# Kernel tuning notes

Measured on AMD Instinct MI355X. Metric: run time of the kernel, lower is better.

Reference implementation:

```python
import jax, jax.numpy as jnp
import numpy as np

B, S = 4, 16384
D_IN, D_HID, D_KEY, D_VAL, N_HEADS = 512, 2048, 64, 64, 8
SEG_FULL, SAMP = 2048, 4
SEG = SEG_FULL // SAMP  # 512: MoD capacity per segment, also attn segment_len


def setup_inputs() -> dict:
    key = jax.random.key(0)
    ks = jax.random.split(key, 10)
    sc = lambda i, shape: (jax.random.normal(ks[i], shape, jnp.float32) * 0.02)
    return {
        "x": jax.random.normal(ks[0], (B, S, D_IN), jnp.float32),
        "w_samp": sc(1, (D_IN, 1)), "b_samp": jnp.zeros((1,), jnp.float32),
        "w_q": sc(2, (D_IN, N_HEADS * D_KEY)),
        "w_k": sc(3, (D_IN, N_HEADS * D_KEY)),
        "w_v": sc(4, (D_IN, N_HEADS * D_VAL)),
        "w_o": sc(5, (N_HEADS * D_VAL, D_IN)),
        "betas": jax.random.normal(ks[6], (1, N_HEADS, 1, D_VAL), jnp.float32),
        "w1": sc(7, (D_IN, D_HID)), "b1": jnp.zeros((D_HID,), jnp.float32),
        "w2": sc(8, (D_HID, D_IN)), "b2": jnp.zeros((D_IN,), jnp.float32),
    }


def _cm_attention(x, w_q, w_k, w_v, w_o, betas):
    """CompressiveMemory: segment-recurrent linear-attn memory + local softmax attn."""
    b, n, _ = x.shape
    nseg = n // SEG

    def split(w, dh):
        y = (x @ w).reshape(b, n, N_HEADS, dh).transpose(0, 2, 1, 3)          # [b,H,n,dh]
        return y.reshape(b, N_HEADS, nseg, SEG, dh).transpose(2, 0, 1, 3, 4)  # [nseg,b,H,SEG,dh]

    qs, ks_, vs = split(w_q, D_KEY), split(w_k, D_KEY), split(w_v, D_VAL)
    gate = jax.nn.sigmoid(betas)                                              # [1,H,1,dv]
    mem0 = jnp.zeros((b, N_HEADS, D_KEY, D_VAL), x.dtype)
    z0 = jnp.ones((b, N_HEADS, D_KEY, 1), x.dtype) / D_KEY
    scale = D_KEY ** -0.5

    def step(carry, seg):
        mem, z = carry
        q, k, v = seg
        sq = jax.nn.elu(q) + 1.0
        sk = jax.nn.elu(k) + 1.0
        scores = jnp.einsum('bhqk,bhsk->bhqs', q, k) * scale
        att_dot = jax.nn.softmax(scores, axis=-1) @ v                         # [b,H,SEG,dv]
        att_mem = (sq @ mem) / (sq @ z)                                       # uses pre-update mem,z
        mem = mem + jnp.einsum('bhsk,bhsv->bhkv', sk, v)                      # linear update
        z = z + sk.sum(axis=-2)[..., None]
        att = gate * att_mem + (1.0 - gate) * att_dot
        return (mem, z), att

    _, outs = jax.lax.scan(step, (mem0, z0), (qs, ks_, vs))                   # [nseg,b,H,SEG,dv]
    out = outs.transpose(1, 0, 3, 2, 4).reshape(b, n, N_HEADS * D_VAL)
    return out @ w_o


def reference(x, w_samp, b_samp, w_q, w_k, w_v, w_o, betas, w1, b1, w2, b2):
    b, s, d = x.shape
    nseg = s // SEG_FULL
    scores = (x @ w_samp + b_samp)[..., 0]                                    # [B,S]
    # top-SEG tokens per full segment (training-mode routing), kept in sequence order
    seg_scores = scores.reshape(b, nseg, SEG_FULL)
    top = jnp.argsort(-seg_scores, axis=-1)[:, :, :SEG]                       # [B,nseg,SEG]
    sel = jnp.sort(top, axis=-1) + (jnp.arange(nseg) * SEG_FULL)[None, :, None]
    flat = sel.reshape(b, nseg * SEG)                                         # global indices, [B,Ssel]
    x_sel = jnp.take_along_axis(x, flat[..., None], axis=1)                   # gather [B,Ssel,D]
    h = _cm_attention(x_sel, w_q, w_k, w_v, w_o, betas)
    h = jax.nn.gelu(h @ w1 + b1, approximate=False) @ w2 + b2                 # MLP (dropout=0)
    bi = jnp.arange(b)[:, None]
    x_out = x.at[bi, flat].add(h)                                             # scatter-add back
    mask = jnp.zeros((b, s), x.dtype).at[bi, flat].set(1.0)
    # faithful to source: zero positions >= number of selected tokens
    pad = (jnp.arange(s)[None, :] < mask.sum(axis=1)[:, None]).astype(x.dtype)
    x_out = x_out * pad[..., None]
    return x_out, mask.reshape(-1, 1), scores.reshape(-1, 1)
```

## Files before the change

### kernel.cpp

```cpp
#include <hip/hip_runtime.h>
#include <math.h>

#define S_TOT 16384
#define BATCH 4
#define DIN 512
#define NH 8
#define DK 64
#define SEGF 2048
#define SEGS 512
#define NSEG 8
#define NUSE 2
#define MROWS (BATCH*NUSE*SEGS)

typedef unsigned int u32;
typedef __attribute__((ext_vector_type(8))) short short8;
typedef __attribute__((ext_vector_type(4))) float f32x4;

__device__ __forceinline__ short f2b(float f) {
  u32 u = __float_as_uint(f);
  u32 r = u + 0x7fffu + ((u >> 16) & 1u);
  return (short)(r >> 16);
}
__device__ __forceinline__ float b2f(short s) {
  return __uint_as_float(((u32)(unsigned short)s) << 16);
}

__global__ __launch_bounds__(256) void scores_transpose(
    const float* __restrict__ x, const float* __restrict__ w,
    const float* __restrict__ bsamp, float* __restrict__ out,
    const float* __restrict__ w_q, const float* __restrict__ w_k,
    const float* __restrict__ w_v, const float* __restrict__ w_o,
    const float* __restrict__ w1,  const float* __restrict__ w2,
    short* __restrict__ Wtqkv, short* __restrict__ Wob,
    short* __restrict__ Wt1,   short* __restrict__ Wt2)
{
  __shared__ float t[32][33];
  int tid = threadIdx.x;
  if (blockIdx.x < 16384) {
    int tok  = blockIdx.x * 4 + (tid >> 6);
    int lane = tid & 63;
    const float4* xr = (const float4*)(x + (size_t)tok * DIN);
    const float4* wr = (const float4*)w;
    float4 a0 = xr[lane],      w0 = wr[lane];
    float4 a1 = xr[lane + 64], w1v = wr[lane + 64];
    float p = a0.x*w0.x + a0.y*w0.y + a0.z*w0.z + a0.w*w0.w
            + a1.x*w1v.x + a1.y*w1v.y + a1.z*w1v.z + a1.w*w1v.w;
    #pragma unroll
    for (int off = 32; off > 0; off >>= 1) p += __shfl_down(p, off);
    if (lane == 0) out[tok] = p + bsamp[0];
    return;
  }
  int bid = blockIdx.x - 16384;
  int txx = tid & 31, ty = tid >> 5;
  if (bid >= 768 && bid < 1024) {
    int tIdx = bid - 768;
    int n0 = (tIdx & 15) * 32, k0 = (tIdx >> 4) * 32;
    #pragma unroll
    for (int r = 0; r < 4; ++r) {
      size_t idx = (size_t)(k0 + ty + 8*r) * 512 + n0 + txx;
      Wob[idx] = f2b(w_o[idx]);
    }
    return;
  }
  const float* src; short* dst; int K, N, rowoff, tIdx;
  if (bid < 768) {
    K = 512; N = 512; tIdx = bid & 255;
    int which = bid >> 8;
    src = which == 0 ? w_q : which == 1 ? w_k : w_v;
    dst = Wtqkv;
    rowoff = which * 512;
  } else if (bid < 2048) {
    K = 512; N = 2048; tIdx = bid - 1024; src = w1; dst = Wt1; rowoff = 0;
  } else {
    K = 2048; N = 512; tIdx = bid - 2048; src = w2; dst = Wt2; rowoff = 0;
  }
  int ntN = N >> 5;
  int n0 = (tIdx % ntN) * 32, k0 = (tIdx / ntN) * 32;
  #pragma unroll
  for (int r = 0; r < 4; ++r)
    t[ty + 8*r][txx] = src[(size_t)(k0 + ty + 8*r) * N + n0 + txx];
  __syncthreads();
  #pragma unroll
  for (int r = 0; r < 4; ++r)
    dst[(size_t)(rowoff + n0 + ty + 8*r) * K + k0 + txx] = f2b(t[txx][ty + 8*r]);
}

__global__ __launch_bounds__(1024) void topk_rank(
    const float* __restrict__ scores, int* __restrict__ flags,
    float* __restrict__ maskOut)
{
  int c = blockIdx.x & 7, g = (blockIdx.x >> 3) & 7, b = blockIdx.x >> 6;
  __shared__ float sc[SEGF];
  __shared__ int pcnt[3][256];
  int tid = threadIdx.x;
  const float* src = scores + (size_t)b*S_TOT + (size_t)g*SEGF;
  *(float2*)&sc[tid*2] = *(const float2*)(src + tid*2);
  __syncthreads();
  int e = tid & 255;
  int q = tid >> 8;
  int i0 = c*256 + e;
  float mine = sc[i0];
  int cnt = 0;
  int j0 = q * 512;
  #pragma unroll 2
  for (int j = j0; j < j0 + 512; j += 8) {
    float4 a = *(const float4*)&sc[j];
    float4 d = *(const float4*)&sc[j + 4];
    cnt += (a.x > mine || (a.x == mine && (j+0) < i0)) ? 1 : 0;
    cnt += (a.y > mine || (a.y == mine && (j+1) < i0)) ? 1 : 0;
    cnt += (a.z > mine || (a.z == mine && (j+2) < i0)) ? 1 : 0;
    cnt += (a.w > mine || (a.w == mine && (j+3) < i0)) ? 1 : 0;
    cnt += (d.x > mine || (d.x == mine && (j+4) < i0)) ? 1 : 0;
    cnt += (d.y > mine || (d.y == mine && (j+5) < i0)) ? 1 : 0;
    cnt += (d.z > mine || (d.z == mine && (j+6) < i0)) ? 1 : 0;
    cnt += (d.w > mine || (d.w == mine && (j+7) < i0)) ? 1 : 0;
  }
  if (q) pcnt[q-1][e] = cnt;
  __syncthreads();
  if (q == 0) {
    cnt += pcnt[0][e] + pcnt[1][e] + pcnt[2][e];
    int flg = (cnt < SEGS) ? 1 : 0;
    flags[(((b << 3) + g) << 11) + i0] = flg;
    maskOut[(size_t)b*S_TOT + (size_t)g*SEGF + i0] = flg ? 1.0f : 0.0f;
  }
}

__global__ __launch_bounds__(256) void topk_compact(
    const int* __restrict__ flags, int* __restrict__ flat, int* __restrict__ inv)
{
  int g = blockIdx.x & 1, b = blockIdx.x >> 1;
  __shared__ int wsum[4];
  int tid = threadIdx.x;
  int lane = tid & 63, w = tid >> 6;
  const int* f = flags + (((b << 3) + g) << 11);
  int fl[8]; int ls = 0;
  #pragma unroll
  for (int l = 0; l < 8; ++l) { fl[l] = f[tid*8 + l]; ls += fl[l]; }
  int inc = ls;
  #pragma unroll
  for (int off = 1; off < 64; off <<= 1) {
    int t = __shfl_up(inc, off);
    if (lane >= off) inc += t;
  }
  if (lane == 63) wsum[w] = inc;
  __syncthreads();
  int base = 0;
  #pragma unroll
  for (int ww = 0; ww < 4; ++ww) base += (ww < w) ? wsum[ww] : 0;
  int pos = base + inc - ls;
  #pragma unroll
  for (int l = 0; l < 8; ++l) {
    int i = tid*8 + l;
    inv[b*(NUSE*SEGF) + g*SEGF + i] = fl[l] ? (g*SEGS + pos) : -1;
    if (fl[l]) {
      flat[b*(NSEG*SEGS) + g*SEGS + pos] = g*SEGF + i;
      pos++;
    }
  }
}

__global__ __launch_bounds__(256) void gather_cast(
    const float* __restrict__ x, const int* __restrict__ flat,
    short* __restrict__ xsel)
{
  int tok  = blockIdx.x * 4 + (threadIdx.x >> 6);
  int lane = threadIdx.x & 63;
  int b = tok >> 10, i = tok & 1023;
  int gidx = flat[b * (NSEG*SEGS) + i];
  const float* srcp = x + ((size_t)(b * S_TOT + gidx)) * DIN + lane*8;
  float4 a0 = *(const float4*)srcp;
  float4 a1 = *(const float4*)(srcp + 4);
  uint4 o;
  o.x = (u32)(unsigned short)f2b(a0.x) | ((u32)(unsigned short)f2b(a0.y) << 16);
  o.y = (u32)(unsigned short)f2b(a0.z) | ((u32)(unsigned short)f2b(a0.w) << 16);
  o.z = (u32)(unsigned short)f2b(a1.x) | ((u32)(unsigned short)f2b(a1.y) << 16);
  o.w = (u32)(unsigned short)f2b(a1.z) | ((u32)(unsigned short)f2b(a1.w) << 16);
  *(uint4*)(xsel + (size_t)tok * DIN + lane*8) = o;
}

template<int BM, int BN, int WM, int WN, int BK>
__global__ __launch_bounds__(256) void gemm_bf16(
    const short* __restrict__ A, const short* __restrict__ Bt,
    const float* __restrict__ bias, float* __restrict__ Cf,
    short* __restrict__ Cb, short* __restrict__ VtOut, short* __restrict__ KtOut,
    int M, int N, int K, int act)
{
  constexpr int WAVES_N = BN / WN;
  constexpr int FM = WM / 16, FN = WN / 16;
  constexpr int RPB = BK / 8;
  __shared__ short Al[2][BM * BK];
  __shared__ short Bl[2][BN * BK];
  const int tid = threadIdx.x;
  const int lane = tid & 63, wid = tid >> 6;
  const int wr = wid / WAVES_N, wc = wid % WAVES_N;
  const int bm = blockIdx.y * BM, bn = blockIdx.x * BN;
  const int ln15 = lane & 15, hi8 = (lane >> 4) * 8;

  f32x4 acc[FM][FN];
  #pragma unroll
  for (int i = 0; i < FM; ++i)
    #pragma unroll
    for (int j = 0; j < FN; ++j)
      #pragma unroll
      for (int e = 0; e < 4; ++e) acc[i][j][e] = 0.f;

  const int NT = K / BK;

  auto stage = [&](int t, int buf) {
    const int k0 = t * BK;
    #pragma unroll
    for (int i = 0; i < BM*BK/2048; ++i) {
      int slot = i*256 + tid;
      int row = slot / RPB, col = (slot % RPB) * 8;
      const short* gp = A + (size_t)(bm + row) * K + k0 + col;
      __builtin_amdgcn_global_load_lds(
          (const __attribute__((address_space(1))) void*)gp,
          (__attribute__((address_space(3))) void*)&Al[buf][row*BK + col],
          16, 0, 0);
    }
    #pragma unroll
    for (int i = 0; i < BN*BK/2048; ++i) {
      int slot = i*256 + tid;
      int row = slot / RPB, col = (slot % RPB) * 8;
      const short* gp = Bt + (size_t)(bn + row) * K + k0 + col;
      __builtin_amdgcn_global_load_lds(
          (const __attribute__((address_space(1))) void*)gp,
          (__attribute__((address_space(3))) void*)&Bl[buf][row*BK + col],
          16, 0, 0);
    }
  };

  stage(0, 0);
  __syncthreads();
  int cur = 0;
  for (int t = 0; t < NT; ++t) {
    if (t + 1 < NT) stage(t + 1, cur ^ 1);
    #pragma unroll
    for (int ks = 0; ks < BK/32; ++ks) {
      short8 af[FM], bf_[FN];
      #pragma unroll
      for (int fm = 0; fm < FM; ++fm)
        af[fm] = *(const short8*)&Al[cur][(wr*WM + fm*16 + ln15)*BK + ks*32 + hi8];
      #pragma unroll
      for (int fn = 0; fn < FN; ++fn)
        bf_[fn] = *(const short8*)&Bl[cur][(wc*WN + fn*16 + ln15)*BK + ks*32 + hi8];
      #pragma unroll
      for (int fm = 0; fm < FM; ++fm)
        #pragma unroll
        for (int fn = 0; fn < FN; ++fn)
          acc[fm][fn] = __builtin_amdgcn_mfma_f32_16x16x32_bf16(af[fm], bf_[fn], acc[fm][fn], 0, 0, 0);
    }
    __syncthreads();
    cur ^= 1;
  }

  const int crow0 = (lane >> 4) * 4, ccol = lane & 15;
  #pragma unroll
  for (int fm = 0; fm < FM; ++fm) {
    #pragma unroll
    for (int fn = 0; fn < FN; ++fn) {
      int c = bn + wc*WN + fn*16 + ccol;
      int r0 = bm + wr*WM + fm*16 + crow0;
      float vv[4];
      #pragma unroll
      for (int j = 0; j < 4; ++j) {
        float v = acc[fm][fn][j];
        if (bias) v += bias[c];
        if (act == 1) v = 0.5f * v * (1.0f + erff(v * 0.70710678118f));
        vv[j] = v;
        if (Cf) Cf[(size_t)(r0 + j) * N + c] = v;
        if (Cb) Cb[(size_t)(r0 + j) * N + c] = f2b(v);
      }
      if (VtOut && c >= 1024) {
        int hh = (c - 1024) >> 6, dv = c & 63;
        int bb = r0 >> 10, key = r0 & 1023;
        u32 lo = (u32)(unsigned short)f2b(vv[0]) | ((u32)(unsigned short)f2b(vv[1]) << 16);
        u32 hi = (u32)(unsigned short)f2b(vv[2]) | ((u32)(unsigned short)f2b(vv[3]) << 16);
        *(uint2*)&VtOut[((size_t)((bb*8 + hh)*64 + dv) << 10) + key] = make_uint2(lo, hi);
      }
      if (KtOut && c >= 512 && c < 1024) {
        int hh = (c - 512) >> 6, dk = c & 63;
        int bb = r0 >> 10, key = r0 & 1023;
        float e0 = vv[0] > 0.f ? vv[0] + 1.f : __expf(vv[0]);
        float e1 = vv[1] > 0.f ? vv[1] + 1.f : __expf(vv[1]);
        float e2 = vv[2] > 0.f ? vv[2] + 1.f : __expf(vv[2]);
        float e3 = vv[3] > 0.f ? vv[3] + 1.f : __expf(vv[3]);
        u32 lo = (u32)(unsigned short)f2b(e0) | ((u32)(unsigned short)f2b(e1) << 16);
        u32 hi = (u32)(unsigned short)f2b(e2) | ((u32)(unsigned short)f2b(e3) << 16);
        *(uint2*)&KtOut[((size_t)((bb*8 + hh)*64 + dk) << 10) + key] = make_uint2(lo, hi);
      }
    }
  }
}

__global__ __launch_bounds__(256) void memsum_mfma(
    const short* __restrict__ Kt, const short* __restrict__ Vt,
    short* __restrict__ m0t, float* __restrict__ zf)
{
  int b = blockIdx.x >> 3, h = blockIdx.x & 7;
  const short* ktb = Kt + ((size_t)((b*8+h)*64) << 10);
  const short* vtb = Vt + ((size_t)((b*8+h)*64) << 10);
  int tid = threadIdx.x, lane = tid & 63, w = tid >> 6;
  int ln15 = lane & 15, hi8 = (lane >> 4) * 8;
  f32x4 acc[4];
  #pragma unroll
  for (int nf = 0; nf < 4; ++nf) acc[nf] = (f32x4){0.f,0.f,0.f,0.f};
  #pragma unroll 4
  for (int ks = 0; ks < 16; ++ks) {
    short8 a = *(const short8*)&vtb[(size_t)(w*16 + ln15)*1024 + ks*32 + hi8];
    #pragma unroll
    for (int nf = 0; nf < 4; ++nf) {
      short8 bfr = *(const short8*)&ktb[(size_t)(nf*16 + ln15)*1024 + ks*32 + hi8];
      acc[nf] = __builtin_amdgcn_mfma_f32_16x16x32_bf16(a, bfr, acc[nf], 0, 0, 0);
    }
  }
  size_t mb = (size_t)(b*NH + h) * 4096;
  #pragma unroll
  for (int nf = 0; nf < 4; ++nf)
    #pragma unroll
    for (int j = 0; j < 4; ++j)
      m0t[mb + (size_t)(w*16 + (lane>>4)*4 + j)*64 + nf*16 + ln15] = f2b(acc[nf][j]);
  int row = tid >> 2, q = tid & 3;
  float zs = 0.f;
  #pragma unroll 4
  for (int i = 0; i < 16; ++i) {
    short8 kv = *(const short8*)&ktb[(size_t)row*1024 + q*128 + i*8];
    #pragma unroll
    for (int e = 0; e < 8; ++e) zs += b2f(kv[e]);
  }
  zs += __shfl_xor(zs, 1); zs += __shfl_xor(zs, 2);
  if (q == 0) zf[(b*8+h)*64 + row] = 0.015625f + zs;
}

__global__ __launch_bounds__(256) void attn4(
    const short* __restrict__ qkv, const short* __restrict__ vt,
    const short* __restrict__ m0t, const float* __restrict__ zf,
    const float* __restrict__ betas, short* __restrict__ att)
{
  __shared__ short Ks[128*64];
  __shared__ short Vts[64*128];
  __shared__ short Ps[4*16*128];
  __shared__ float zl[64];
  __shared__ float relay[64];
  int tid = threadIdx.x, lane = tid & 63, w = tid >> 6;
  int ln15 = lane & 15, hi8 = (lane >> 4) * 8;
  int bx = blockIdx.x;
  int qt = bx & 7, h = (bx >> 3) & 7, g = (bx >> 6) & 1, b = bx >> 7;
  const int seg0 = b*1024 + g*512;
  const int qbase = seg0 + qt*64;

  short8 qf[2];
  {
    const short* qg = qkv + (size_t)(qbase + w*16 + ln15)*1536 + h*64;
    qf[0] = *(const short8*)(qg + hi8);
    qf[1] = *(const short8*)(qg + 32 + hi8);
  }
  if (g && tid < 16) *(float4*)&zl[tid*4] = *(const float4*)(zf + (size_t)(b*8+h)*64 + tid*4);

  const short* kg = qkv + (size_t)seg0*1536 + 512 + h*64;
  const short* vg = vt + ((size_t)((b*8+h)*64) << 10) + g*512;
  short* Pw = &Ps[w*2048];

  f32x4 oacc[4];
  #pragma unroll
  for (int nf = 0; nf < 4; ++nf) oacc[nf] = (f32x4){0.f,0.f,0.f,0.f};
  float lsum[4] = {0.f,0.f,0.f,0.f};

  for (int c = 0; c < 4; ++c) {
    __syncthreads();
    #pragma unroll
    for (int p = 0; p < 4; ++p) {
      int slot = p*256 + tid;
      int row = slot >> 3;
      int off = ((slot & 7)*8) ^ ((row & 7)*8);
      __builtin_amdgcn_global_load_lds(
        (const __attribute__((address_space(1))) void*)(kg + (size_t)(c*128 + row)*1536 + off),
        (__attribute__((address_space(3))) void*)&Ks[slot*8], 16, 0, 0);
    }
    #pragma unroll
    for (int p = 0; p < 4; ++p) {
      int slot = p*256 + tid;
      int row = slot >> 4;
      int off = ((slot & 15)*8) ^ ((row & 7)*8);
      __builtin_amdgcn_global_load_lds(
        (const __attribute__((address_space(1))) void*)(vg + ((size_t)row << 10) + c*128 + off),
        (__attribute__((address_space(3))) void*)&Vts[slot*8], 16, 0, 0);
    }
    __syncthreads();

    f32x4 sf[8];
    #pragma unroll
    for (int nf = 0; nf < 8; ++nf) sf[nf] = (f32x4){0.f,0.f,0.f,0.f};
    __builtin_amdgcn_s_setprio(1);
    #pragma unroll
    for (int ks = 0; ks < 2; ++ks)
      #pragma unroll
      for (int nf = 0; nf < 8; ++nf) {
        int row = nf*16 + ln15;
        short8 kb = *(const short8*)&Ks[row*64 + ((ks*32 + hi8) ^ ((row&7)*8))];
        sf[nf] = __builtin_amdgcn_mfma_f32_16x16x32_bf16(qf[ks], kb, sf[nf], 0, 0, 0);
      }
    __builtin_amdgcn_s_setprio(0);
    #pragma unroll
    for (int nf = 0; nf < 8; ++nf)
      #pragma unroll
      for (int j = 0; j < 4; ++j) {
        float p = __expf(sf[nf][j] * 0.125f);
        lsum[j] += p;
        int q = (lane >> 4)*4 + j;
        int key = nf*16 + ln15;
        Pw[q*128 + (key ^ ((q&7)*8))] = f2b(p);
      }
    __builtin_amdgcn_s_setprio(1);
    #pragma unroll
    for (int ks = 0; ks < 4; ++ks) {
      short8 pa = *(const short8*)&Pw[ln15*128 + ((ks*32 + hi8) ^ ((ln15&7)*8))];
      #pragma unroll
      for (int nf = 0; nf < 4; ++nf) {
        int row = nf*16 + ln15;
        short8 vb = *(const short8*)&Vts[row*128 + ((ks*32 + hi8) ^ ((row&7)*8))];
        oacc[nf] = __builtin_amdgcn_mfma_f32_16x16x32_bf16(pa, vb, oacc[nf], 0, 0, 0);
      }
    }
    __builtin_amdgcn_s_setprio(0);
  }

  float linv[4];
  #pragma unroll
  for (int j = 0; j < 4; ++j) {
    float s = lsum[j];
    s += __shfl_xor(s, 1); s += __shfl_xor(s, 2);
    s += __shfl_xor(s, 4); s += __shfl_xor(s, 8);
    linv[j] = 1.f / s;
  }

  f32x4 mfr[4];
  #pragma unroll
  for (int nf = 0; nf < 4; ++nf) mfr[nf] = (f32x4){0.f,0.f,0.f,0.f};
  float dinv[4] = {0.f,0.f,0.f,0.f};
  if (g) {
    __syncthreads();
    const short* mg = m0t + (size_t)(b*8+h)*4096;
    #pragma unroll
    for (int p = 0; p < 2; ++p) {
      int slot = p*256 + tid;
      int row = slot >> 3;
      int off = ((slot & 7)*8) ^ ((row & 7)*8);
      __builtin_amdgcn_global_load_lds(
        (const __attribute__((address_space(1))) void*)(mg + (size_t)row*64 + off),
        (__attribute__((address_space(3))) void*)&Ks[slot*8], 16, 0, 0);
    }
    __syncthreads();
    float sqv[2][8]; short8 sqf[2];
    #pragma unroll
    for (int ks = 0; ks < 2; ++ks)
      #pragma unroll
      for (int e = 0; e < 8; ++e) {
        float f = b2f(qf[ks][e]);
        f = f > 0.f ? f + 1.f : __expf(f);
        sqv[ks][e] = f; sqf[ks][e] = f2b(f);
      }
    float denp = 0.f;
    #pragma unroll
    for (int ks = 0; ks < 2; ++ks)
      #pragma unroll
      for (int e = 0; e < 8; ++e) denp += sqv[ks][e] * zl[ks*32 + hi8 + e];
    denp += __shfl_xor(denp, 16); denp += __shfl_xor(denp, 32);
    if (lane < 16) relay[w*16 + lane] = denp;
    #pragma unroll
    for (int ks = 0; ks < 2; ++ks)
      #pragma unroll
      for (int nf = 0; nf < 4; ++nf) {
        int row = nf*16 + ln15;
        short8 mb_ = *(const short8*)&Ks[row*64 + ((ks*32 + hi8) ^ ((row&7)*8))];
        mfr[nf] = __builtin_amdgcn_mfma_f32_16x16x32_bf16(sqf[ks], mb_, mfr[nf], 0, 0, 0);
      }
    #pragma unroll
    for (int j = 0; j < 4; ++j)
      dinv[j] = 1.f / relay[w*16 + (lane>>4)*4 + j];
  }

  #pragma unroll
  for (int nf = 0; nf < 4; ++nf) {
    float bt = betas[h*64 + nf*16 + ln15];
    float gt = 1.f / (1.f + __expf(-bt));
    #pragma unroll
    for (int j = 0; j < 4; ++j) {
      float ad = oacc[nf][j] * linv[j];
      float v = g ? (gt * mfr[nf][j] * dinv[j] + (1.f - gt) * ad) : (1.f - gt) * ad;
      int qrow = qbase + w*16 + (lane>>4)*4 + j;
      att[(size_t)qrow*512 + h*64 + nf*16 + ln15] = f2b(v);
    }
  }
}

__global__ __launch_bounds__(256) void final_kernel(
    const float* __restrict__ x, const int* __restrict__ inv,
    const float* __restrict__ hm, float* __restrict__ outX)
{
  int row  = blockIdx.x * 4 + (threadIdx.x >> 6);
  int lane = threadIdx.x & 63;
  int b = row >> 14;
  int s = row & (S_TOT - 1);
  size_t base = (size_t)row * DIN + lane * 8;
  if (s >= NUSE * SEGF) {
    float4 z = make_float4(0.f,0.f,0.f,0.f);
    *(float4*)(outX + base)     = z;
    *(float4*)(outX + base + 4) = z;
    return;
  }
  float4 a0 = *(const float4*)(x + base);
  float4 a1 = *(const float4*)(x + base + 4);
  int i = inv[b * (NUSE*SEGF) + s];
  if (i >= 0) {
    size_t hb = (size_t)(b * (NUSE*SEGS) + i) * DIN + lane * 8;
    float4 h0 = *(const float4*)(hm + hb);
    float4 h1 = *(const float4*)(hm + hb + 4);
    a0.x += h0.x; a0.y += h0.y; a0.z += h0.z; a0.w += h0.w;
    a1.x += h1.x; a1.y += h1.y; a1.z += h1.z; a1.w += h1.w;
  }
  *(float4*)(outX + base)     = a0;
  *(float4*)(outX + base + 4) = a1;
}

extern "C" void kernel_launch(void* const* d_in, const int* in_sizes, int n_in,
                              void* d_out, int out_size, void* d_ws, size_t ws_size,
                              hipStream_t stream) {
  (void)in_sizes; (void)n_in; (void)out_size; (void)ws_size;
  const float* x      = (const float*)d_in[0];
  const float* w_samp = (const float*)d_in[1];
  const float* b_samp = (const float*)d_in[2];
  const float* w_q    = (const float*)d_in[3];
  const float* w_k    = (const float*)d_in[4];
  const float* w_v    = (const float*)d_in[5];
  const float* w_o    = (const float*)d_in[6];
  const float* betas  = (const float*)d_in[7];
  const float* w1     = (const float*)d_in[8];
  const float* b1     = (const float*)d_in[9];
  const float* w2     = (const float*)d_in[10];
  const float* b2     = (const float*)d_in[11];

  float* outX      = (float*)d_out;
  float* outMask   = outX + (size_t)BATCH * S_TOT * DIN;
  float* outScores = outMask + (size_t)BATCH * S_TOT;

  char* ws = (char*)d_ws;
  int*   flat  = (int*)(ws);
  int*   inv   = (int*)(ws + 65536);
  int*   flags = (int*)(ws + 131072);
  short* M0t   = (short*)(ws + 393216);
  float* Zf    = (float*)(ws + 655360);
  short* Wtqkv = (short*)(ws + 1048576);
  short* Wob   = (short*)(ws + 2621440);
  short* Wt1   = (short*)(ws + 3145728);
  short* Wt2   = (short*)(ws + 5242880);
  short* xsel  = (short*)(ws + 7340032);
  short* qkv   = (short*)(ws + 11534336);
  short* Vt    = (short*)(ws + 24117248);
  short* attb  = (short*)(ws + 28311552);
  short* Kt    = (short*)(ws + 36700160);
  short* WfT   = (short*)(ws + 40894464);
  short* hidB  = (short*)(ws + 7340032);
  float* Hf    = (float*)(ws + 24117248);

  scores_transpose<<<16384 + 3072, 256, 0, stream>>>(
      x, w_samp, b_samp, outScores,
      w_q, w_k, w_v, w_o, w1, w2, Wtqkv, Wob, Wt1, Wt2);
  topk_rank<<<BATCH*NSEG*8, 1024, 0, stream>>>(outScores, flags, outMask);
  topk_compact<<<BATCH*NUSE, 256, 0, stream>>>(flags, flat, inv);

  gemm_bf16<64,64,32,32,64><<<dim3(8,32), 256, 0, stream>>>(
      Wt1, Wob, nullptr, nullptr, WfT, nullptr, nullptr, 2048, 512, 512, 0);

  gather_cast<<<MROWS/4, 256, 0, stream>>>(x, flat, xsel);

  gemm_bf16<128,128,64,64,32><<<dim3(12,32), 256, 0, stream>>>(
      xsel, Wtqkv, nullptr, nullptr, qkv, Vt, Kt, MROWS, 1536, 512, 0);

  memsum_mfma<<<BATCH*NH, 256, 0, stream>>>(Kt, Vt, M0t, Zf);
  attn4<<<512, 256, 0, stream>>>(qkv, Vt, M0t, Zf, betas, attb);

  gemm_bf16<128,128,64,64,32><<<dim3(16,32), 256, 0, stream>>>(
      attb, WfT, b1, nullptr, hidB, nullptr, nullptr, MROWS, 2048, 512, 1);
  gemm_bf16<64,64,32,32,64><<<dim3(8,64), 256, 0, stream>>>(
      hidB, Wt2, b2, Hf, nullptr, nullptr, nullptr, MROWS, 512, 2048, 0);

  final_kernel<<<(BATCH*S_TOT)/4, 256, 0, stream>>>(x, inv, Hf, outX);
}
```

Measured before the change: 218.8 us.

## Fuse residual scatter into final GEMM and memory summary into attention

Removes the separate final_kernel and Hf buffer. The last MLP GEMM now writes x plus h directly into the output rows given by the gather indices, and the gather kernel copies unselected rows and zeroes padded rows. It also removes the memsum_mfma launch by having each second-segment attention block recompute the per-head memory matrix and normalizer from Kt/Vt into LDS. This saves launches and a full-size pass over the intermediate, but the memory matrix is now computed redundantly by 8 query-tile blocks per head, and the epilogue does scattered, per-element residual reads.

Result: slower. 227.9 us (+4.2%).

```diff
diff --git a/kernel.cpp b/kernel.cpp
--- a/kernel.cpp
+++ b/kernel.cpp
@@ -159,23 +159,41 @@
   }
 }
 
-__global__ __launch_bounds__(256) void gather_cast(
+__global__ __launch_bounds__(256) void gather_base(
     const float* __restrict__ x, const int* __restrict__ flat,
-    short* __restrict__ xsel)
+    const int* __restrict__ inv, short* __restrict__ xsel,
+    float* __restrict__ outX)
 {
-  int tok  = blockIdx.x * 4 + (threadIdx.x >> 6);
-  int lane = threadIdx.x & 63;
-  int b = tok >> 10, i = tok & 1023;
-  int gidx = flat[b * (NSEG*SEGS) + i];
-  const float* srcp = x + ((size_t)(b * S_TOT + gidx)) * DIN + lane*8;
-  float4 a0 = *(const float4*)srcp;
-  float4 a1 = *(const float4*)(srcp + 4);
-  uint4 o;
-  o.x = (u32)(unsigned short)f2b(a0.x) | ((u32)(unsigned short)f2b(a0.y) << 16);
-  o.y = (u32)(unsigned short)f2b(a0.z) | ((u32)(unsigned short)f2b(a0.w) << 16);
-  o.z = (u32)(unsigned short)f2b(a1.x) | ((u32)(unsigned short)f2b(a1.y) << 16);
-  o.w = (u32)(unsigned short)f2b(a1.z) | ((u32)(unsigned short)f2b(a1.w) << 16);
-  *(uint4*)(xsel + (size_t)tok * DIN + lane*8) = o;
+  int tid = threadIdx.x;
+  int lane = tid & 63;
+  if (blockIdx.x < 1024) {
+    int tok = blockIdx.x * 4 + (tid >> 6);
+    int b = tok >> 10, i = tok & 1023;
+    int gidx = flat[b * (NSEG*SEGS) + i];
+    const float* srcp = x + ((size_t)(b * S_TOT + gidx)) * DIN + lane*8;
+    float4 a0 = *(const float4*)srcp;
+    float4 a1 = *(const float4*)(srcp + 4);
+    uint4 o;
+    o.x = (u32)(unsigned short)f2b(a0.x) | ((u32)(unsigned short)f2b(a0.y) << 16);
+    o.y = (u32)(unsigned short)f2b(a0.z) | ((u32)(unsigned short)f2b(a0.w) << 16);
+    o.z = (u32)(unsigned short)f2b(a1.x) | ((u32)(unsigned short)f2b(a1.y) << 16);
+    o.w = (u32)(unsigned short)f2b(a1.z) | ((u32)(unsigned short)f2b(a1.w) << 16);
+    *(uint4*)(xsel + (size_t)tok * DIN + lane*8) = o;
+    return;
+  }
+  int row = (blockIdx.x - 1024) * 4 + (tid >> 6);
+  int b = row >> 14;
+  int s = row & (S_TOT - 1);
+  size_t base = (size_t)row * DIN + lane * 8;
+  if (s >= NUSE * SEGF) {
+    float4 z = make_float4(0.f,0.f,0.f,0.f);
+    *(float4*)(outX + base)     = z;
+    *(float4*)(outX + base + 4) = z;
+    return;
+  }
+  if (inv[b * (NUSE*SEGF) + s] >= 0) return;
+  *(float4*)(outX + base)     = *(const float4*)(x + base);
+  *(float4*)(outX + base + 4) = *(const float4*)(x + base + 4);
 }
 
 template<int BM, int BN, int WM, int WN, int BK>
@@ -183,6 +201,7 @@
     const short* __restrict__ A, const short* __restrict__ Bt,
     const float* __restrict__ bias, float* __restrict__ Cf,
     short* __restrict__ Cb, short* __restrict__ VtOut, short* __restrict__ KtOut,
+    const float* __restrict__ xres, const int* __restrict__ gflat,
     int M, int N, int K, int act)
 {
   constexpr int WAVES_N = BN / WN;
@@ -257,10 +276,17 @@
   const int crow0 = (lane >> 4) * 4, ccol = lane & 15;
   #pragma unroll
   for (int fm = 0; fm < FM; ++fm) {
+    int r0 = bm + wr*WM + fm*16 + crow0;
+    int toks[4];
+    if (xres) {
+      int bb2 = r0 >> 10;
+      #pragma unroll
+      for (int j = 0; j < 4; ++j)
+        toks[j] = bb2 * S_TOT + gflat[bb2 * (NSEG*SEGS) + ((r0 + j) & 1023)];
+    }
     #pragma unroll
     for (int fn = 0; fn < FN; ++fn) {
       int c = bn + wc*WN + fn*16 + ccol;
-      int r0 = bm + wr*WM + fm*16 + crow0;
       float vv[4];
       #pragma unroll
       for (int j = 0; j < 4; ++j) {
@@ -268,8 +294,13 @@
         if (bias) v += bias[c];
         if (act == 1) v = 0.5f * v * (1.0f + erff(v * 0.70710678118f));
         vv[j] = v;
-        if (Cf) Cf[(size_t)(r0 + j) * N + c] = v;
-        if (Cb) Cb[(size_t)(r0 + j) * N + c] = f2b(v);
+        if (xres) {
+          size_t o = (size_t)toks[j] * DIN + c;
+          Cf[o] = xres[o] + v;
+        } else {
+          if (Cf) Cf[(size_t)(r0 + j) * N + c] = v;
+          if (Cb) Cb[(size_t)(r0 + j) * N + c] = f2b(v);
+        }
       }
       if (VtOut && c >= 1024) {
         int hh = (c - 1024) >> 6, dv = c & 63;
@@ -293,49 +324,10 @@
   }
 }
 
-__global__ __launch_bounds__(256) void memsum_mfma(
-    const short* __restrict__ Kt, const short* __restrict__ Vt,
-    short* __restrict__ m0t, float* __restrict__ zf)
-{
-  int b = blockIdx.x >> 3, h = blockIdx.x & 7;
-  const short* ktb = Kt + ((size_t)((b*8+h)*64) << 10);
-  const short* vtb = Vt + ((size_t)((b*8+h)*64) << 10);
-  int tid = threadIdx.x, lane = tid & 63, w = tid >> 6;
-  int ln15 = lane & 15, hi8 = (lane >> 4) * 8;
-  f32x4 acc[4];
-  #pragma unroll
-  for (int nf = 0; nf < 4; ++nf) acc[nf] = (f32x4){0.f,0.f,0.f,0.f};
-  #pragma unroll 4
-  for (int ks = 0; ks < 16; ++ks) {
-    short8 a = *(const short8*)&vtb[(size_t)(w*16 + ln15)*1024 + ks*32 + hi8];
-    #pragma unroll
-    for (int nf = 0; nf < 4; ++nf) {
-      short8 bfr = *(const short8*)&ktb[(size_t)(nf*16 + ln15)*1024 + ks*32 + hi8];
-      acc[nf] = __builtin_amdgcn_mfma_f32_16x16x32_bf16(a, bfr, acc[nf], 0, 0, 0);
-    }
-  }
-  size_t mb = (size_t)(b*NH + h) * 4096;
-  #pragma unroll
-  for (int nf = 0; nf < 4; ++nf)
-    #pragma unroll
-    for (int j = 0; j < 4; ++j)
-      m0t[mb + (size_t)(w*16 + (lane>>4)*4 + j)*64 + nf*16 + ln15] = f2b(acc[nf][j]);
-  int row = tid >> 2, q = tid & 3;
-  float zs = 0.f;
-  #pragma unroll 4
-  for (int i = 0; i < 16; ++i) {
-    short8 kv = *(const short8*)&ktb[(size_t)row*1024 + q*128 + i*8];
-    #pragma unroll
-    for (int e = 0; e < 8; ++e) zs += b2f(kv[e]);
-  }
-  zs += __shfl_xor(zs, 1); zs += __shfl_xor(zs, 2);
-  if (q == 0) zf[(b*8+h)*64 + row] = 0.015625f + zs;
-}
-
 __global__ __launch_bounds__(256) void attn4(
     const short* __restrict__ qkv, const short* __restrict__ vt,
-    const short* __restrict__ m0t, const float* __restrict__ zf,
-    const float* __restrict__ betas, short* __restrict__ att)
+    const short* __restrict__ kt, const float* __restrict__ betas,
+    short* __restrict__ att)
 {
   __shared__ short Ks[128*64];
   __shared__ short Vts[64*128];
@@ -355,10 +347,24 @@
     qf[0] = *(const short8*)(qg + hi8);
     qf[1] = *(const short8*)(qg + 32 + hi8);
   }
-  if (g && tid < 16) *(float4*)&zl[tid*4] = *(const float4*)(zf + (size_t)(b*8+h)*64 + tid*4);
+
+  const short* ktb = kt + ((size_t)((b*8+h)*64) << 10);
+  const short* vtb = vt + ((size_t)((b*8+h)*64) << 10);
+  if (g) {
+    int zrow = tid >> 2, zq = tid & 3;
+    float zs = 0.f;
+    #pragma unroll 4
+    for (int i = 0; i < 16; ++i) {
+      short8 kv = *(const short8*)&ktb[(size_t)zrow*1024 + zq*128 + i*8];
+      #pragma unroll
+      for (int e2 = 0; e2 < 8; ++e2) zs += b2f(kv[e2]);
+    }
+    zs += __shfl_xor(zs, 1); zs += __shfl_xor(zs, 2);
+    if (zq == 0) zl[zrow] = 0.015625f + zs;
+  }
 
   const short* kg = qkv + (size_t)seg0*1536 + 512 + h*64;
-  const short* vg = vt + ((size_t)((b*8+h)*64) << 10) + g*512;
+  const short* vg = vtb + g*512;
   short* Pw = &Ps[w*2048];
 
   f32x4 oacc[4];
@@ -440,16 +446,26 @@
   float dinv[4] = {0.f,0.f,0.f,0.f};
   if (g) {
     __syncthreads();
-    const short* mg = m0t + (size_t)(b*8+h)*4096;
-    #pragma unroll
-    for (int p = 0; p < 2; ++p) {
-      int slot = p*256 + tid;
-      int row = slot >> 3;
-      int off = ((slot & 7)*8) ^ ((row & 7)*8);
-      __builtin_amdgcn_global_load_lds(
-        (const __attribute__((address_space(1))) void*)(mg + (size_t)row*64 + off),
-        (__attribute__((address_space(3))) void*)&Ks[slot*8], 16, 0, 0);
-    }
+    f32x4 macc[4];
+    #pragma unroll
+    for (int nf = 0; nf < 4; ++nf) macc[nf] = (f32x4){0.f,0.f,0.f,0.f};
+    #pragma unroll 4
+    for (int ks = 0; ks < 16; ++ks) {
+      short8 a = *(const short8*)&vtb[(size_t)(w*16 + ln15)*1024 + ks*32 + hi8];
+      #pragma unroll
+      for (int nf = 0; nf < 4; ++nf) {
+        short8 bb = *(const short8*)&ktb[(size_t)(nf*16 + ln15)*1024 + ks*32 + hi8];
+        macc[nf] = __builtin_amdgcn_mfma_f32_16x16x32_bf16(a, bb, macc[nf], 0, 0, 0);
+      }
+    }
+    #pragma unroll
+    for (int nf = 0; nf < 4; ++nf)
+      #pragma unroll
+      for (int j = 0; j < 4; ++j) {
+        int dvr = w*16 + (lane>>4)*4 + j;
+        int dkc = nf*16 + ln15;
+        Ks[dvr*64 + (dkc ^ ((dvr&7)*8))] = f2b(macc[nf][j]);
+      }
     __syncthreads();
     float sqv[2][8]; short8 sqf[2];
     #pragma unroll
@@ -492,35 +508,6 @@
       att[(size_t)qrow*512 + h*64 + nf*16 + ln15] = f2b(v);
     }
   }
-}
-
-__global__ __launch_bounds__(256) void final_kernel(
-    const float* __restrict__ x, const int* __restrict__ inv,
-    const float* __restrict__ hm, float* __restrict__ outX)
-{
-  int row  = blockIdx.x * 4 + (threadIdx.x >> 6);
-  int lane = threadIdx.x & 63;
-  int b = row >> 14;
-  int s = row & (S_TOT - 1);
-  size_t base = (size_t)row * DIN + lane * 8;
-  if (s >= NUSE * SEGF) {
-    float4 z = make_float4(0.f,0.f,0.f,0.f);
-    *(float4*)(outX + base)     = z;
-    *(float4*)(outX + base + 4) = z;
-    return;
-  }
-  float4 a0 = *(const float4*)(x + base);
-  float4 a1 = *(const float4*)(x + base + 4);
-  int i = inv[b * (NUSE*SEGF) + s];
-  if (i >= 0) {
-    size_t hb = (size_t)(b * (NUSE*SEGS) + i) * DIN + lane * 8;
-    float4 h0 = *(const float4*)(hm + hb);
-    float4 h1 = *(const float4*)(hm + hb + 4);
-    a0.x += h0.x; a0.y += h0.y; a0.z += h0.z; a0.w += h0.w;
-    a1.x += h1.x; a1.y += h1.y; a1.z += h1.z; a1.w += h1.w;
-  }
-  *(float4*)(outX + base)     = a0;
-  *(float4*)(outX + base + 4) = a1;
 }
 
 extern "C" void kernel_launch(void* const* d_in, const int* in_sizes, int n_in,
@@ -548,8 +535,6 @@
   int*   flat  = (int*)(ws);
   int*   inv   = (int*)(ws + 65536);
   int*   flags = (int*)(ws + 131072);
-  short* M0t   = (short*)(ws + 393216);
-  float* Zf    = (float*)(ws + 655360);
   short* Wtqkv = (short*)(ws + 1048576);
   short* Wob   = (short*)(ws + 2621440);
   short* Wt1   = (short*)(ws + 3145728);
@@ -561,7 +546,6 @@
   short* Kt    = (short*)(ws + 36700160);
   short* WfT   = (short*)(ws + 40894464);
   short* hidB  = (short*)(ws + 7340032);
-  float* Hf    = (float*)(ws + 24117248);
 
   scores_transpose<<<16384 + 3072, 256, 0, stream>>>(
       x, w_samp, b_samp, outScores,
@@ -570,20 +554,21 @@
   topk_compact<<<BATCH*NUSE, 256, 0, stream>>>(flags, flat, inv);
 
   gemm_bf16<64,64,32,32,64><<<dim3(8,32), 256, 0, stream>>>(
-      Wt1, Wob, nullptr, nullptr, WfT, nullptr, nullptr, 2048, 512, 512, 0);
-
-  gather_cast<<<MROWS/4, 256, 0, stream>>>(x, flat, xsel);
+      Wt1, Wob, nullptr, nullptr, WfT, nullptr, nullptr, nullptr, nullptr,
+      2048, 512, 512, 0);
+
+  gather_base<<<1024 + 16384, 256, 0, stream>>>(x, flat, inv, xsel, outX);
 
   gemm_bf16<128,128,64,64,32><<<dim3(12,32), 256, 0, stream>>>(
-      xsel, Wtqkv, nullptr, nullptr, qkv, Vt, Kt, MROWS, 1536, 512, 0);
-
-  memsum_mfma<<<BATCH*NH, 256, 0, stream>>>(Kt, Vt, M0t, Zf);
-  attn4<<<512, 256, 0, stream>>>(qkv, Vt, M0t, Zf, betas, attb);
+      xsel, Wtqkv, nullptr, nullptr, qkv, Vt, Kt, nullptr, nullptr,
+      MROWS, 1536, 512, 0);
+
+  attn4<<<512, 256, 0, stream>>>(qkv, Vt, Kt, betas, attb);
 
   gemm_bf16<128,128,64,64,32><<<dim3(16,32), 256, 0, stream>>>(
-      attb, WfT, b1, nullptr, hidB, nullptr, nullptr, MROWS, 2048, 512, 1);
+      attb, WfT, b1, nullptr, hidB, nullptr, nullptr, nullptr, nullptr,
+      MROWS, 2048, 512, 1);
   gemm_bf16<64,64,32,32,64><<<dim3(8,64), 256, 0, stream>>>(
-      hidB, Wt2, b2, Hf, nullptr, nullptr, nullptr, MROWS, 512, 2048, 0);
-
-  final_kernel<<<(BATCH*S_TOT)/4, 256, 0, stream>>>(x, inv, Hf, outX);
-}
+      hidB, Wt2, b2, outX, nullptr, nullptr, nullptr, x, flat,
+      MROWS, 512, 2048, 0);
+}
```
